# Performance work log

Hardware: AMD Instinct MI355X
Metric: run time of the kernel (lower is better)

The kernel has to match this reference:

```python
import jax, jax.numpy as jnp
import numpy as np

EMBED = 1024
HEADS = 16
HEAD_DIM = EMBED // HEADS
SCALE = HEAD_DIM ** -0.5


def setup_inputs() -> dict:
    key = jax.random.key(0)
    ks = jax.random.split(key, 9)
    init = lambda k, shape: jax.random.normal(k, shape, dtype=jnp.float32) * 0.02
    return {
        "hidden_states": jax.random.normal(ks[0], (32, 257, EMBED), dtype=jnp.float32),
        "Wq": init(ks[1], (EMBED, EMBED)), "bq": init(ks[2], (EMBED,)),
        "Wk": init(ks[3], (EMBED, EMBED)), "bk": init(ks[4], (EMBED,)),
        "Wv": init(ks[5], (EMBED, EMBED)), "bv": init(ks[6], (EMBED,)),
        "Wo": init(ks[7], (EMBED, EMBED)), "bo": init(ks[8], (EMBED,)),
    }


def reference(hidden_states, Wq, bq, Wk, bk, Wv, bv, Wo, bo):
    b, t, d = hidden_states.shape
    # projections (torch Linear: x @ W.T + b); scale applied to Q
    q = (hidden_states @ Wq.T + bq) * SCALE
    k = hidden_states @ Wk.T + bk
    v = hidden_states @ Wv.T + bv
    # [b, h, t, hd]
    q = q.reshape(b, t, HEADS, HEAD_DIM).transpose(0, 2, 1, 3)
    k = k.reshape(b, t, HEADS, HEAD_DIM).transpose(0, 2, 1, 3)
    v = v.reshape(b, t, HEADS, HEAD_DIM).transpose(0, 2, 1, 3)
    # attention scores + softmax (dropout p is a no-op in eval mode)
    scores = jnp.einsum("bhqd,bhkd->bhqk", q, k)
    probs = jax.nn.softmax(scores, axis=-1)
    ctx = jnp.einsum("bhqk,bhkd->bhqd", probs, v)
    ctx = ctx.transpose(0, 2, 1, 3).reshape(b, t, d)
    return ctx @ Wo.T + bo
```

## Files before the change

kernel.cpp:

```cpp
#include <hip/hip_runtime.h>


#define B_   32
#define T_   257
#define TP   272
#define H_   16
#define HD_  64
#define D_   1024
#define NTOK 8224
#define BH_  512
#define FRAG_PER_BH 17408

typedef __bf16 bf16;
typedef __bf16 bf16x4 __attribute__((ext_vector_type(4)));
typedef __bf16 bf16x8 __attribute__((ext_vector_type(8)));
typedef short  s16x4  __attribute__((ext_vector_type(4)));
typedef short  s16x8  __attribute__((ext_vector_type(8)));
typedef float  floatx4 __attribute__((ext_vector_type(4)));

static constexpr size_t SZ_XB   = (size_t)NTOK * D_ * 2;
static constexpr size_t SZ_WQKV = (size_t)3 * D_ * D_ * 2;
static constexpr size_t SZ_W    = (size_t)D_ * D_ * 2;
static constexpr size_t SZ_QK   = (size_t)BH_ * FRAG_PER_BH * 2;

static constexpr size_t OFF_XB   = 0;
static constexpr size_t OFF_WQKV = OFF_XB + SZ_XB;
static constexpr size_t OFF_WO   = OFF_WQKV + SZ_WQKV;
static constexpr size_t OFF_Q    = OFF_WO + SZ_W;
static constexpr size_t OFF_K    = OFF_Q + SZ_QK;
static constexpr size_t OFF_V    = OFF_K + SZ_QK;
static constexpr size_t OFF_CTX  = OFF_V + SZ_QK;

#define GLD16(gp, lp)                                                        \
  __builtin_amdgcn_global_load_lds(                                          \
      (const __attribute__((address_space(1))) void*)(gp),                   \
      (__attribute__((address_space(3))) void*)(lp), 16, 0, 0)

__global__ void cast_bf16_kernel(const float* __restrict__ src,
                                 bf16* __restrict__ dst, int n4) {
  int i = blockIdx.x * blockDim.x + threadIdx.x;
  int stride = gridDim.x * blockDim.x;
  for (int idx = i; idx < n4; idx += stride) {
    float4 v = reinterpret_cast<const float4*>(src)[idx];
    bf16x4 o;
    o[0] = (bf16)v.x; o[1] = (bf16)v.y; o[2] = (bf16)v.z; o[3] = (bf16)v.w;
    reinterpret_cast<bf16x4*>(dst)[idx] = o;
  }
}

__global__ void cast4_kernel(const float* __restrict__ s0, const float* __restrict__ s1,
                             const float* __restrict__ s2, const float* __restrict__ s3,
                             bf16* __restrict__ d0, bf16* __restrict__ d1,
                             bf16* __restrict__ d2, bf16* __restrict__ d3, int n4) {
  const float* s = (blockIdx.y == 0) ? s0 : (blockIdx.y == 1) ? s1
                   : (blockIdx.y == 2) ? s2 : s3;
  bf16* d = (blockIdx.y == 0) ? d0 : (blockIdx.y == 1) ? d1
            : (blockIdx.y == 2) ? d2 : d3;
  int i = blockIdx.x * blockDim.x + threadIdx.x;
  int stride = gridDim.x * blockDim.x;
  for (int idx = i; idx < n4; idx += stride) {
    float4 v = reinterpret_cast<const float4*>(s)[idx];
    bf16x4 o;
    o[0] = (bf16)v.x; o[1] = (bf16)v.y; o[2] = (bf16)v.z; o[3] = (bf16)v.w;
    reinterpret_cast<bf16x4*>(d)[idx] = o;
  }
}



#define PH_MFMA(ACC, AF, BF)                                                 \
  do {                                                                       \
    __builtin_amdgcn_s_setprio(1);                                           \
    _Pragma("unroll") for (int mi_ = 0; mi_ < 4; mi_++)                      \
      _Pragma("unroll") for (int nj_ = 0; nj_ < 2; nj_++)                    \
        _Pragma("unroll") for (int ks_ = 0; ks_ < 2; ks_++)                  \
          ACC[mi_][nj_] = __builtin_amdgcn_mfma_f32_16x16x32_bf16(           \
              AF[mi_][ks_], BF[nj_][ks_], ACC[mi_][nj_], 0, 0, 0);           \
    __builtin_amdgcn_s_setprio(0);                                           \
  } while (0)

#define READ_A(BASE)                                                         \
  do {                                                                       \
    _Pragma("unroll") for (int mi_ = 0; mi_ < 4; mi_++)                      \
      _Pragma("unroll") for (int ks_ = 0; ks_ < 2; ks_++)                    \
        af[mi_][ks_] = *reinterpret_cast<const bf16x8*>(                     \
            smem + (BASE) + aoffs[mi_][ks_]);                                \
  } while (0)

#define READ_B(DST, BASE)                                                    \
  do {                                                                       \
    _Pragma("unroll") for (int nj_ = 0; nj_ < 2; nj_++)                      \
      _Pragma("unroll") for (int ks_ = 0; ks_ < 2; ks_++)                    \
        DST[nj_][ks_] = *reinterpret_cast<const bf16x8*>(                    \
            smem + (BASE) + boffs[nj_][ks_]);                                \
  } while (0)

#define LGKM0                                                                \
  do {                                                                       \
    asm volatile("s_waitcnt lgkmcnt(0)" ::: "memory");                       \
    __builtin_amdgcn_sched_barrier(0);                                       \
  } while (0)

#define TILE4(TT, BB, BBN)                                                   \
  do {                                                                       \
    const int kt1_ = ((TT) + 1 < 16) ? (TT) + 1 : 15;                        \
    const int kt2_ = ((TT) + 2 < 16) ? (TT) + 2 : 15;                        \
    READ_A((BB) * 16384);                                                    \
    READ_B(bf0, 32768 + (BB) * 16384);                                       \
    stageA(BBN, 1, kt1_);                                                    \
    __builtin_amdgcn_s_barrier();                                            \
    LGKM0;                                                                   \
    PH_MFMA(acc00, af, bf0);                                                 \
    __builtin_amdgcn_s_barrier();                                            \
    READ_B(bf1, 32768 + (BB) * 16384 + 8192);                                \
    stageB(BBN, 0, kt1_);                                                    \
    __builtin_amdgcn_s_barrier();                                            \
    LGKM0;                                                                   \
    PH_MFMA(acc01, af, bf1);                                                 \
    __builtin_amdgcn_s_barrier();                                            \
    READ_A((BB) * 16384 + 8192);                                             \
    stageA(BB, 0, kt2_);                                                     \
    __builtin_amdgcn_s_barrier();                                            \
    LGKM0;                                                                   \
    PH_MFMA(acc11, af, bf1);                                                 \
    __builtin_amdgcn_s_barrier();                                            \
    stageB(BB, 1, kt2_);                                                     \
    __builtin_amdgcn_s_barrier();                                            \
    __builtin_amdgcn_sched_barrier(0);                                       \
    PH_MFMA(acc10, af, bf0);                                                 \
    asm volatile("s_waitcnt vmcnt(4)" ::: "memory");                         \
    __builtin_amdgcn_s_barrier();                                            \
  } while (0)

#define EPI_WRITE(ACC_MH0, ACC_MH1, NH)                                      \
  do {                                                                       \
    float bv_[2];                                                            \
    bv_[0] = bias[znb + (NH) * 128 + wc2 * 32 + n15];                        \
    bv_[1] = bias[znb + (NH) * 128 + wc2 * 32 + 16 + n15];                   \
    _Pragma("unroll") for (int mi_ = 0; mi_ < 4; mi_++)                      \
      _Pragma("unroll") for (int nj_ = 0; nj_ < 2; nj_++)                    \
        _Pragma("unroll") for (int r_ = 0; r_ < 4; r_++) {                   \
          int rowL_ = wr2 * 64 + mi_ * 16 + quad * 4 + r_;                   \
          int colL_ = wc2 * 32 + nj_ * 16 + n15;                             \
          smem[rowL_ * 136 + colL_] =                                        \
              (bf16)((ACC_MH0[mi_][nj_][r_] + bv_[nj_]) * scale);            \
          smem[(128 + rowL_) * 136 + colL_] =                                \
              (bf16)((ACC_MH1[mi_][nj_][r_] + bv_[nj_]) * scale);            \
        }                                                                    \
  } while (0)

__global__ __launch_bounds__(512, 2) void qkv_gemm(
    const bf16* __restrict__ xb, const bf16* __restrict__ wqkv,
    const float* __restrict__ bq, const float* __restrict__ bk,
    const float* __restrict__ bv,
    bf16* __restrict__ Qf, bf16* __restrict__ Kf, bf16* __restrict__ Vf) {
  __shared__ bf16 smem[65536];

  const int linear = blockIdx.x;
  const int mt = linear / 12, nt = linear % 12;
  const int m0 = mt * 256, n0 = nt * 256;
  const int tid = threadIdx.x;
  const int lane = tid & 63, w = tid >> 6;
  const int n15 = lane & 15, quad = lane >> 4;
  const int wr2 = w >> 2, wc2 = w & 3;
  const int srow = lane >> 3, sseg = lane & 7;

  auto stageA = [&](int buf, int half, int kt) {
#pragma unroll
    for (int c = 0; c < 2; c++) {
      int r = (w * 2 + c) * 8 + srow;
      int gm = m0 + half * 128 + r; if (gm > NTOK - 1) gm = NTOK - 1;
      int sg = (sseg ^ srow) * 8;
      GLD16(xb + (size_t)gm * D_ + kt * 64 + sg,
            smem + buf * 16384 + half * 8192 + (w * 2 + c) * 512);
    }
  };
  auto stageB = [&](int buf, int half, int kt) {
#pragma unroll
    for (int c = 0; c < 2; c++) {
      int r = (w * 2 + c) * 8 + srow;
      int gn = n0 + half * 128 + r;
      int sg = (sseg ^ srow) * 8;
      GLD16(wqkv + (size_t)gn * D_ + kt * 64 + sg,
            smem + 32768 + buf * 16384 + half * 8192 + (w * 2 + c) * 512);
    }
  };

  int aoffs[4][2], boffs[2][2];
#pragma unroll
  for (int mi = 0; mi < 4; mi++)
#pragma unroll
    for (int ks = 0; ks < 2; ks++) {
      int rh = wr2 * 64 + mi * 16 + n15;
      aoffs[mi][ks] = rh * 64 + ((ks * 4 + quad) ^ (n15 & 7)) * 8;
    }
#pragma unroll
  for (int nj = 0; nj < 2; nj++)
#pragma unroll
    for (int ks = 0; ks < 2; ks++) {
      int rh = wc2 * 32 + nj * 16 + n15;
      boffs[nj][ks] = rh * 64 + ((ks * 4 + quad) ^ (n15 & 7)) * 8;
    }

  floatx4 acc00[4][2] = {}, acc01[4][2] = {}, acc10[4][2] = {}, acc11[4][2] = {};
  bf16x8 af[4][2], bf0[2][2], bf1[2][2];

  stageA(0, 0, 0); stageB(0, 0, 0); stageA(0, 1, 0); stageB(0, 1, 0);
  stageA(1, 0, 1); stageB(1, 1, 1);
  asm volatile("s_waitcnt vmcnt(4)" ::: "memory");
  __builtin_amdgcn_s_barrier();

  for (int t = 0; t < 16; t += 2) {
    TILE4(t, 0, 1);
    TILE4(t + 1, 1, 0);
  }

  asm volatile("s_waitcnt vmcnt(0)" ::: "memory");
  __builtin_amdgcn_s_barrier();

  const int z = nt >> 2;
  bf16* zdst = (z == 0) ? Qf : (z == 1) ? Kf : Vf;
  const float scale = (z == 0) ? 0.125f : 1.0f;
  const float* bias = (z == 0) ? bq : (z == 1) ? bk : bv;
  const int znb = (nt & 3) * 256;

  const int mEnd = (m0 + 256 < NTOK) ? m0 + 256 : NTOK;
  const int span = mEnd - m0;
  const int bA = m0 / T_;
  const int tA = m0 - bA * T_;
  const int tEndA = (tA + span < T_) ? tA + span : T_;
  const int tgA0 = tA >> 4;
  const int nA = ((tEndA - 1) >> 4) - tgA0 + 1;
  int nU = nA, tEndB = 0;
  if (tA + span > T_ && bA + 1 < B_) {
    tEndB = tA + span - T_;
    nU += ((tEndB - 1) >> 4) + 1;
  }

  auto epi_store = [&](int nh_) {
    const int h0 = (nt & 3) * 4 + nh_ * 2;
    for (int u = w; u < nU * 2; u += 8) {
      int g = u >> 1, hh = u & 1;
      int bb, tg, tlo, thi;
      if (g < nA) {
        bb = bA; tg = tgA0 + g;
        tlo = (tA > tg * 16) ? tA : tg * 16;
        int te = tg * 16 + 16; thi = (te < tEndA) ? te : tEndA;
      } else {
        bb = bA + 1; tg = g - nA; tlo = tg * 16;
        int te = tg * 16 + 16; thi = (te < tEndB) ? te : tEndB;
      }
      bf16* gb = zdst + (size_t)(bb * H_ + h0 + hh) * FRAG_PER_BH + tg * 1024;
      const int hc = hh * 64;
      if (z != 2) {
        int ki = lane & 15, dc = lane >> 4;
        int tt = tg * 16 + ki;
        if (tt >= tlo && tt < thi) {
          int rowL = bb * T_ + tt - m0;
          bf16x8 v0 = *reinterpret_cast<const bf16x8*>(smem + rowL * 136 + hc + dc * 8);
          bf16x8 v1 = *reinterpret_cast<const bf16x8*>(smem + rowL * 136 + hc + 32 + dc * 8);
          *reinterpret_cast<bf16x8*>(gb + dc * 128 + ki * 8) = v0;
          *reinterpret_cast<bf16x8*>(gb + 512 + dc * 128 + ki * 8) = v1;
        }
      } else {
        int q2 = (lane >> 4) & 3, d16 = lane & 15;
        int tb = tg * 16 + q2 * 4;
        bool full = (tb >= tlo) && (tb + 3 < thi);
#pragma unroll
        for (int p = 0; p < 2; p++) {
          bf16x8 vv;
#pragma unroll
          for (int dp = 0; dp < 2; dp++)
#pragma unroll
            for (int ki = 0; ki < 4; ki++) {
              int tt = tb + ki;
              int rr = (bb * T_ + tt - m0) & 255;
              vv[dp * 4 + ki] = smem[rr * 136 + hc + p * 32 + dp * 16 + d16];
            }
          bf16* cp = gb + (p * 4 + q2) * 128 + d16 * 8;
          if (full) {
            *reinterpret_cast<bf16x8*>(cp) = vv;
          } else {
#pragma unroll
            for (int dp = 0; dp < 2; dp++)
#pragma unroll
              for (int ki = 0; ki < 4; ki++) {
                int tt = tb + ki;
                if (tt >= tlo && tt < thi) cp[dp * 4 + ki] = vv[dp * 4 + ki];
              }
          }
        }
      }
    }
  };

  EPI_WRITE(acc00, acc10, 0);
  __syncthreads();
  epi_store(0);
  __syncthreads();
  EPI_WRITE(acc01, acc11, 1);
  __syncthreads();
  epi_store(1);
}

__global__ __launch_bounds__(256) void attn_kernel(
    const bf16* __restrict__ Qf, const bf16* __restrict__ Kf,
    const bf16* __restrict__ Vf, bf16* __restrict__ ctx) {
  __shared__ bf16 smem[34816];

  const int bh = blockIdx.x;
  const int tid = threadIdx.x;
  const int lane = tid & 63, w = tid >> 6;
  const int n15 = lane & 15, quad = lane >> 4;
  const int b = bh >> 4, h = bh & 15;

  const bf16* Qb = Qf + (size_t)bh * FRAG_PER_BH;
  const bf16* Kb = Kf + (size_t)bh * FRAG_PER_BH;
  const bf16* Vb = Vf + (size_t)bh * FRAG_PER_BH;

#pragma unroll
  for (int j = 0; j < 17; j++) {
    int c = w * 17 + j;
    const bf16* src = (c < 34) ? (Kb + c * 512) : (Vb + (c - 34) * 512);
    GLD16(src + lane * 8, smem + c * 512);
  }
  __syncthreads();
  const bf16* Ksh = smem;
  const bf16* Vsh = smem + 17408;

  const int fo = quad * 128 + n15 * 8;

  for (int qt = w; qt < 17; qt += 4) {
    bf16x8 qb0 = *reinterpret_cast<const bf16x8*>(Qb + qt * 1024 + fo);
    bf16x8 qb1 = *reinterpret_cast<const bf16x8*>(Qb + qt * 1024 + 512 + fo);

    floatx4 s[17];
#pragma unroll
    for (int kt = 0; kt < 17; kt++) {
      bf16x8 ka0 = *reinterpret_cast<const bf16x8*>(Ksh + kt * 1024 + fo);
      bf16x8 ka1 = *reinterpret_cast<const bf16x8*>(Ksh + kt * 1024 + 512 + fo);
      floatx4 c = {};
      c = __builtin_amdgcn_mfma_f32_16x16x32_bf16(ka0, qb0, c, 0, 0, 0);
      c = __builtin_amdgcn_mfma_f32_16x16x32_bf16(ka1, qb1, c, 0, 0, 0);
      s[kt] = c;
    }
    s[16][1] = -1e30f; s[16][2] = -1e30f; s[16][3] = -1e30f;
    if (quad != 0) s[16][0] = -1e30f;

    float m0 = -1e30f;
#pragma unroll
    for (int kt = 0; kt < 17; kt++)
#pragma unroll
      for (int r = 0; r < 4; r++) m0 = fmaxf(m0, s[kt][r]);
    m0 = fmaxf(m0, __shfl_xor(m0, 16));
    m0 = fmaxf(m0, __shfl_xor(m0, 32));

    float sum = 0.f;
    s16x4 pb[17];
#pragma unroll
    for (int kt = 0; kt < 17; kt++) {
      bf16x4 ph;
#pragma unroll
      for (int r = 0; r < 4; r++) {
        float p = __expf(s[kt][r] - m0);
        sum += p;
        ph[r] = (bf16)p;
      }
      pb[kt] = __builtin_bit_cast(s16x4, ph);
    }
    sum += __shfl_xor(sum, 16);
    sum += __shfl_xor(sum, 32);

    floatx4 o[4] = {};
#pragma unroll
    for (int kt = 0; kt < 17; kt++) {
#pragma unroll
      for (int p = 0; p < 2; p++) {
        bf16x8 vv = *reinterpret_cast<const bf16x8*>(
            Vsh + ((kt * 2 + p) * 4 + quad) * 128 + n15 * 8);
        s16x8 v16 = __builtin_bit_cast(s16x8, vv);
        s16x4 vlo = __builtin_shufflevector(v16, v16, 0, 1, 2, 3);
        s16x4 vhi = __builtin_shufflevector(v16, v16, 4, 5, 6, 7);
        o[p * 2]     = __builtin_amdgcn_mfma_f32_16x16x16bf16_1k(vlo, pb[kt], o[p * 2], 0, 0, 0);
        o[p * 2 + 1] = __builtin_amdgcn_mfma_f32_16x16x16bf16_1k(vhi, pb[kt], o[p * 2 + 1], 0, 0, 0);
      }
    }

    int q = qt * 16 + n15;
    if (q < T_) {
      float inv = 1.0f / sum;
      size_t ob = ((size_t)(b * T_ + q)) * D_ + h * 64 + quad * 4;
#pragma unroll
      for (int dt = 0; dt < 4; dt++) {
        bf16x4 ov;
#pragma unroll
        for (int r = 0; r < 4; r++) ov[r] = (bf16)(o[dt][r] * inv);
        *reinterpret_cast<bf16x4*>(ctx + ob + dt * 16) = ov;
      }
    }
  }
}

__global__ __launch_bounds__(256) void o_gemm(
    const bf16* __restrict__ ctx, const bf16* __restrict__ wo,
    const float* __restrict__ bo, float* __restrict__ out) {
  __shared__ bf16 Ash[128 * 32];
  __shared__ bf16 Bsh[128 * 32];

  const int linear = blockIdx.x;
  const int nbase = (linear & 7) * 128;
  const int mbase = (linear >> 3) * 128;
  const int tid = threadIdx.x;
  const int lane = tid & 63;
  const int w = tid >> 6;
  const int wr = w >> 1, wc = w & 1;
  const int n15 = lane & 15, quad = lane >> 4;

  const int lrow = lane >> 2;
  const int lseg = (lane & 3) * 8;

  floatx4 acc[4][4] = {};

  for (int k0 = 0; k0 < D_; k0 += 32) {
#pragma unroll
    for (int c = 0; c < 2; c++) {
      int r0 = w * 32 + c * 16;
      int row = r0 + lrow;
      int gm = mbase + row; if (gm > NTOK - 1) gm = NTOK - 1;
      GLD16(ctx + (size_t)gm * D_ + k0 + lseg, Ash + r0 * 32);
      GLD16(wo + (size_t)(nbase + row) * D_ + k0 + lseg, Bsh + r0 * 32);
    }
    __syncthreads();
    bf16x8 af[4], bfr[4];
#pragma unroll
    for (int i = 0; i < 4; i++) {
      af[i]  = *reinterpret_cast<const bf16x8*>(Ash + (wr * 64 + i * 16 + n15) * 32 + quad * 8);
      bfr[i] = *reinterpret_cast<const bf16x8*>(Bsh + (wc * 64 + i * 16 + n15) * 32 + quad * 8);
    }
#pragma unroll
    for (int i = 0; i < 4; i++)
#pragma unroll
      for (int j = 0; j < 4; j++)
        acc[i][j] = __builtin_amdgcn_mfma_f32_16x16x32_bf16(af[i], bfr[j], acc[i][j], 0, 0, 0);
    __syncthreads();
  }

#pragma unroll
  for (int i = 0; i < 4; i++) {
    int rowb = mbase + wr * 64 + i * 16 + quad * 4;
#pragma unroll
    for (int j = 0; j < 4; j++) {
      int col = nbase + wc * 64 + j * 16 + n15;
      float bval = bo[col];
#pragma unroll
      for (int r = 0; r < 4; r++) {
        int m = rowb + r;
        if (m < NTOK) out[(size_t)m * D_ + col] = acc[i][j][r] + bval;
      }
    }
  }
}

extern "C" void kernel_launch(void* const* d_in, const int* in_sizes, int n_in,
                              void* d_out, int out_size, void* d_ws, size_t ws_size,
                              hipStream_t stream) {
  const float* hs = (const float*)d_in[0];
  const float* Wq = (const float*)d_in[1];
  const float* bq = (const float*)d_in[2];
  const float* Wk = (const float*)d_in[3];
  const float* bk = (const float*)d_in[4];
  const float* Wv = (const float*)d_in[5];
  const float* bv = (const float*)d_in[6];
  const float* Wo = (const float*)d_in[7];
  const float* bo = (const float*)d_in[8];

  char* ws = (char*)d_ws;
  bf16* xb   = (bf16*)(ws + OFF_XB);
  bf16* wqkv = (bf16*)(ws + OFF_WQKV);
  bf16* wob  = (bf16*)(ws + OFF_WO);
  bf16* Qfw  = (bf16*)(ws + OFF_Q);
  bf16* Kfw  = (bf16*)(ws + OFF_K);
  bf16* Vfw  = (bf16*)(ws + OFF_V);
  bf16* ctx  = (bf16*)(ws + OFF_CTX);

  cast_bf16_kernel<<<2048, 256, 0, stream>>>(hs, xb, NTOK * D_ / 4);
  cast4_kernel<<<dim3(256, 4), 256, 0, stream>>>(
      Wq, Wk, Wv, Wo,
      wqkv, wqkv + (size_t)D_ * D_, wqkv + (size_t)2 * D_ * D_, wob,
      D_ * D_ / 4);

  qkv_gemm<<<396, 512, 0, stream>>>(xb, wqkv, bq, bk, bv, Qfw, Kfw, Vfw);
  attn_kernel<<<BH_, 256, 0, stream>>>(Qfw, Kfw, Vfw, ctx);
  o_gemm<<<520, 256, 0, stream>>>(ctx, wob, bo, (float*)d_out);
}
```

Before: 234.7 us.

## Merge cast kernels and restructure QKV GEMM prefetch schedule

Combines the activation cast and the four weight casts into a single launch with a 2D grid, removing one kernel launch. It also reworks the QKV GEMM main-loop pipeline so that each tile refills its own buffer for k-tile t+2, with all four stage loads issued inside the tile. The prologue now fully prefetches two k-tiles and the vmcnt waits are raised to 8. This changes how global-to-LDS loads overlap with MFMA phases, and the merged cast kernel gives the large activation cast only 512 x-blocks where it previously had 2048.

```diff
diff --git a/kernel.cpp b/kernel.cpp
--- a/kernel.cpp
+++ b/kernel.cpp
@@ -36,26 +36,23 @@
       (const __attribute__((address_space(1))) void*)(gp),                   \
       (__attribute__((address_space(3))) void*)(lp), 16, 0, 0)
 
-__global__ void cast_bf16_kernel(const float* __restrict__ src,
-                                 bf16* __restrict__ dst, int n4) {
-  int i = blockIdx.x * blockDim.x + threadIdx.x;
-  int stride = gridDim.x * blockDim.x;
-  for (int idx = i; idx < n4; idx += stride) {
-    float4 v = reinterpret_cast<const float4*>(src)[idx];
-    bf16x4 o;
-    o[0] = (bf16)v.x; o[1] = (bf16)v.y; o[2] = (bf16)v.z; o[3] = (bf16)v.w;
-    reinterpret_cast<bf16x4*>(dst)[idx] = o;
-  }
-}
-
-__global__ void cast4_kernel(const float* __restrict__ s0, const float* __restrict__ s1,
-                             const float* __restrict__ s2, const float* __restrict__ s3,
-                             bf16* __restrict__ d0, bf16* __restrict__ d1,
-                             bf16* __restrict__ d2, bf16* __restrict__ d3, int n4) {
-  const float* s = (blockIdx.y == 0) ? s0 : (blockIdx.y == 1) ? s1
-                   : (blockIdx.y == 2) ? s2 : s3;
-  bf16* d = (blockIdx.y == 0) ? d0 : (blockIdx.y == 1) ? d1
-            : (blockIdx.y == 2) ? d2 : d3;
+__global__ void cast_all_kernel(const float* __restrict__ hs,
+                                const float* __restrict__ Wq, const float* __restrict__ Wk,
+                                const float* __restrict__ Wv, const float* __restrict__ Wo,
+                                bf16* __restrict__ xb, bf16* __restrict__ wqkv,
+                                bf16* __restrict__ wob) {
+  const int y = blockIdx.y;
+  const float* s;
+  bf16* d;
+  int n4;
+  if (y == 0) {
+    s = hs; d = xb; n4 = NTOK * D_ / 4;
+  } else {
+    int z = y - 1;
+    s = (z == 0) ? Wq : (z == 1) ? Wk : (z == 2) ? Wv : Wo;
+    d = (z < 3) ? wqkv + (size_t)z * D_ * D_ : wob;
+    n4 = D_ * D_ / 4;
+  }
   int i = blockIdx.x * blockDim.x + threadIdx.x;
   int stride = gridDim.x * blockDim.x;
   for (int idx = i; idx < n4; idx += stride) {
@@ -101,34 +98,37 @@
     __builtin_amdgcn_sched_barrier(0);                                       \
   } while (0)
 
-#define TILE4(TT, BB, BBN)                                                   \
-  do {                                                                       \
-    const int kt1_ = ((TT) + 1 < 16) ? (TT) + 1 : 15;                        \
-    const int kt2_ = ((TT) + 2 < 16) ? (TT) + 2 : 15;                        \
+#define TILE4(TT, BB)                                                        \
+  do {                                                                       \
+    const int ktn_ = ((TT) + 2 < 16) ? (TT) + 2 : 15;                        \
+                        \
     READ_A((BB) * 16384);                                                    \
     READ_B(bf0, 32768 + (BB) * 16384);                                       \
-    stageA(BBN, 1, kt1_);                                                    \
+    asm volatile("s_waitcnt lgkmcnt(8)" ::: "memory");                       \
     __builtin_amdgcn_s_barrier();                                            \
     LGKM0;                                                                   \
     PH_MFMA(acc00, af, bf0);                                                 \
     __builtin_amdgcn_s_barrier();                                            \
+          \
     READ_B(bf1, 32768 + (BB) * 16384 + 8192);                                \
-    stageB(BBN, 0, kt1_);                                                    \
+    stageA(BB, 0, ktn_);                                                     \
+    stageB(BB, 0, ktn_);                                                     \
     __builtin_amdgcn_s_barrier();                                            \
     LGKM0;                                                                   \
     PH_MFMA(acc01, af, bf1);                                                 \
     __builtin_amdgcn_s_barrier();                                            \
+                                       \
     READ_A((BB) * 16384 + 8192);                                             \
-    stageA(BB, 0, kt2_);                                                     \
+    stageB(BB, 1, ktn_);                                                     \
     __builtin_amdgcn_s_barrier();                                            \
     LGKM0;                                                                   \
     PH_MFMA(acc11, af, bf1);                                                 \
     __builtin_amdgcn_s_barrier();                                            \
-    stageB(BB, 1, kt2_);                                                     \
-    __builtin_amdgcn_s_barrier();                                            \
+              \
+    stageA(BB, 1, ktn_);                                                     \
     __builtin_amdgcn_sched_barrier(0);                                       \
     PH_MFMA(acc10, af, bf0);                                                 \
-    asm volatile("s_waitcnt vmcnt(4)" ::: "memory");                         \
+    asm volatile("s_waitcnt vmcnt(8)" ::: "memory");                         \
     __builtin_amdgcn_s_barrier();                                            \
   } while (0)
 
@@ -205,14 +205,14 @@
   floatx4 acc00[4][2] = {}, acc01[4][2] = {}, acc10[4][2] = {}, acc11[4][2] = {};
   bf16x8 af[4][2], bf0[2][2], bf1[2][2];
 
-  stageA(0, 0, 0); stageB(0, 0, 0); stageA(0, 1, 0); stageB(0, 1, 0);
-  stageA(1, 0, 1); stageB(1, 1, 1);
-  asm volatile("s_waitcnt vmcnt(4)" ::: "memory");
+  stageA(0, 0, 0); stageB(0, 0, 0); stageB(0, 1, 0); stageA(0, 1, 0);
+  stageA(1, 0, 1); stageB(1, 0, 1); stageB(1, 1, 1); stageA(1, 1, 1);
+  asm volatile("s_waitcnt vmcnt(8)" ::: "memory");
   __builtin_amdgcn_s_barrier();
 
   for (int t = 0; t < 16; t += 2) {
-    TILE4(t, 0, 1);
-    TILE4(t + 1, 1, 0);
+    TILE4(t, 0);
+    TILE4(t + 1, 1);
   }
 
   asm volatile("s_waitcnt vmcnt(0)" ::: "memory");
@@ -483,11 +483,8 @@
   bf16* Vfw  = (bf16*)(ws + OFF_V);
   bf16* ctx  = (bf16*)(ws + OFF_CTX);
 
-  cast_bf16_kernel<<<2048, 256, 0, stream>>>(hs, xb, NTOK * D_ / 4);
-  cast4_kernel<<<dim3(256, 4), 256, 0, stream>>>(
-      Wq, Wk, Wv, Wo,
-      wqkv, wqkv + (size_t)D_ * D_, wqkv + (size_t)2 * D_ * D_, wob,
-      D_ * D_ / 4);
+  cast_all_kernel<<<dim3(512, 5), 256, 0, stream>>>(hs, Wq, Wk, Wv, Wo,
+                                                    xb, wqkv, wob);
 
   qkv_gemm<<<396, 512, 0, stream>>>(xb, wqkv, bq, bk, bv, Qfw, Kfw, Vfw);
   attn_kernel<<<BH_, 256, 0, stream>>>(Qfw, Kfw, Vfw, ctx);
```

New measurement: 236.1 us. About the same (+0.6%).
